# Optimization experiments

Measured on AMD Instinct MI355X. Metric: run time of the kernel, lower is better.

## Reference

```python
import jax, jax.numpy as jnp
import numpy as np

S = 4096
D_MODEL = 1024
D_INTERNAL = 4096


def setup_inputs() -> dict:
    key = jax.random.key(0)
    ks = jax.random.split(key, 12)
    s = 0.02
    return {
        "x": jax.random.normal(ks[0], (S, D_MODEL), dtype=jnp.float32),
        # projection weights stored as [d_in, d_out] so y = x @ W + b
        "Wq": jax.random.normal(ks[1], (D_MODEL, D_MODEL), dtype=jnp.float32) * s,
        "bq": jnp.zeros((D_MODEL,), dtype=jnp.float32),
        "Wk": jax.random.normal(ks[2], (D_MODEL, D_MODEL), dtype=jnp.float32) * s,
        "bk": jnp.zeros((D_MODEL,), dtype=jnp.float32),
        "Wv": jax.random.normal(ks[3], (D_MODEL, D_MODEL), dtype=jnp.float32) * s,
        "bv": jnp.zeros((D_MODEL,), dtype=jnp.float32),
        "W1": jax.random.normal(ks[4], (D_MODEL, D_INTERNAL), dtype=jnp.float32) * s,
        "b1": jnp.zeros((D_INTERNAL,), dtype=jnp.float32),
        "W2": jax.random.normal(ks[5], (D_INTERNAL, D_MODEL), dtype=jnp.float32) * s,
        "b2": jnp.zeros((D_MODEL,), dtype=jnp.float32),
    }


def reference(x, Wq, bq, Wk, bk, Wv, bv, W1, b1, W2, b2):
    # x: [S, D] (module is unbatched: k.transpose(0,1) implies 2-D input)
    d_model = x.shape[-1]
    q = x @ Wq + bq                         # [S, D]
    k = x @ Wk + bk                         # [S, D]
    v = x @ Wv + bv                         # [S, D]
    scores = (q @ k.T) / jnp.sqrt(jnp.asarray(d_model, x.dtype))  # [S, S]
    s = x.shape[0]
    causal = jnp.triu(jnp.ones((s, s), dtype=bool), k=1)           # True above diag
    scores = jnp.where(causal, jnp.asarray(-1e9, x.dtype), scores)
    attn = jax.nn.softmax(scores, axis=-1)  # [S, S]
    attended = attn @ v                     # [S, D]
    h = x + attended                        # residual 1
    ff = jax.nn.relu(h @ W1 + b1) @ W2 + b2 # 2-layer MLP
    out = h + ff                            # residual 2
    return (out, attn)
```

## Files before the change

### kernel.cpp

```cpp
#include <hip/hip_runtime.h>
#include <hip/hip_bf16.h>


typedef __attribute__((ext_vector_type(4))) float  f32x4;
typedef __attribute__((ext_vector_type(8))) short  bf16x8;
typedef __attribute__((ext_vector_type(4))) unsigned short us4;
typedef __attribute__((ext_vector_type(8))) unsigned short us8;

#define DEVINL __device__ __forceinline__

static constexpr int S   = 4096;
static constexpr int DM  = 1024;
static constexpr int DI  = 4096;

DEVINL unsigned short f2bf(float f) {
  union { float f; unsigned u; } v; v.f = f;
  unsigned r = v.u + 0x7fffu + ((v.u >> 16) & 1u);
  return (unsigned short)(r >> 16);
}

DEVINL float bf2f(unsigned short b) {
  union { unsigned u; float f; } v; v.u = ((unsigned)b) << 16;
  return v.f;
}

DEVINL void gld_lds16(const unsigned short* g, unsigned short* l) {
  __builtin_amdgcn_global_load_lds(
      (const __attribute__((address_space(1))) void*)g,
      (__attribute__((address_space(3))) void*)l,
      16, 0, 0);
}

DEVINL int xcd_remap(int orig, int nwg) {
  const int q = nwg >> 3, r = nwg & 7;
  const int x = orig & 7, idx = orig >> 3;
  return (x < r ? x * (q + 1) : r * (q + 1) + (x - r) * q) + idx;
}

__global__ void cvt_f32_bf16(const float* __restrict__ in,
                             unsigned short* __restrict__ out, long n) {
  long i = ((long)blockIdx.x * 256 + threadIdx.x) * 8;
  if (i >= n) return;
  f32x4 a = *(const f32x4*)(in + i);
  f32x4 b = *(const f32x4*)(in + i + 4);
  us8 o;
  o[0] = f2bf(a[0]); o[1] = f2bf(a[1]); o[2] = f2bf(a[2]); o[3] = f2bf(a[3]);
  o[4] = f2bf(b[0]); o[5] = f2bf(b[1]); o[6] = f2bf(b[2]); o[7] = f2bf(b[3]);
  *(us8*)(out + i) = o;
}

__global__ void transpose_cvt(const float* __restrict__ in,
                              unsigned short* __restrict__ out, int R, int C) {
  __shared__ float tile[32][33];
  const int bx = blockIdx.x * 32, by = blockIdx.y * 32;
  const int tx = threadIdx.x, ty = threadIdx.y;
  #pragma unroll
  for (int j = 0; j < 4; ++j) {
    int r = ty + j * 8;
    tile[r][tx] = in[(size_t)(by + r) * C + bx + tx];
  }
  __syncthreads();
  #pragma unroll
  for (int j = 0; j < 4; ++j) {
    int r = ty + j * 8;
    out[(size_t)(bx + r) * R + by + tx] = f2bf(tile[tx][r]);
  }
}

__global__ void transpose_bf16(const unsigned short* __restrict__ in, int ld,
                               unsigned short* __restrict__ out, int ldo) {
  __shared__ unsigned short tile[32][33];
  const int bx = blockIdx.x * 32, by = blockIdx.y * 32;
  const int tx = threadIdx.x, ty = threadIdx.y;
  #pragma unroll
  for (int j = 0; j < 4; ++j) {
    int r = ty + j * 8;
    tile[r][tx] = in[(size_t)(by + r) * ld + bx + tx];
  }
  __syncthreads();
  #pragma unroll
  for (int j = 0; j < 4; ++j) {
    int r = ty + j * 8;
    out[(size_t)(bx + r) * ldo + by + tx] = tile[tx][r];
  }
}

enum { EPI_QKV = 0, EPI_SCE = 1, EPI_FF1 = 4, EPI_PART = 6 };

#define VM_WAIT4 asm volatile("s_waitcnt vmcnt(4)" ::: "memory")
#define VM_WAIT0 asm volatile("s_waitcnt vmcnt(0)" ::: "memory")

template <int EPI, bool TRI_PACK, bool TRI_TRUNC>
__launch_bounds__(256, 3)
__global__ void gemm4(const unsigned short* __restrict__ A,
                      const unsigned short* __restrict__ Bt,
                      int M, int N, int K, int lda, int ldb, int kChunk, int GX,
                      const float* __restrict__ bias,
                      float* __restrict__ Cf,
                      unsigned short* __restrict__ Cb,
                      float scale) {
  const int wgid = xcd_remap(blockIdx.x, gridDim.x);
  int bm, bn;
  if (TRI_PACK) {
    int t = wgid;
    bm = (int)((sqrtf(8.f * (float)t + 1.f) - 1.f) * 0.5f);
    while ((bm + 1) * (bm + 2) / 2 <= t) ++bm;
    while (bm * (bm + 1) / 2 > t) --bm;
    bn = t - bm * (bm + 1) / 2;
  } else { bm = wgid / GX; bn = wgid % GX; }
  const int bm0 = bm * 128, bn0 = bn * 128;

  const int kbeg = blockIdx.z * kChunk;
  int kend = min(K, kbeg + kChunk);
  if (TRI_TRUNC) kend = min(kend, bm0 + 128);
  const int len = kend - kbeg;
  const int NT = (len > 0) ? (len >> 5) : 0;

  __shared__ __align__(16) unsigned short lds[3 * 8192];

  const int tid  = threadIdx.x;
  const int lane = tid & 63;
  const int w    = tid >> 6;
  const int wr   = w >> 1, wc = w & 1;
  const int fr   = lane & 15, fq = lane >> 4;

  f32x4 acc[4][4] = {};

  const int tq = tid >> 2;
  const int swcolE = ((tid & 3) * 8) ^ ((tq & 6) << 2);
  const unsigned short* gA = A  + (size_t)(bm0 + tq) * lda + kbeg + swcolE;
  const unsigned short* gB = Bt + (size_t)(bn0 + tq) * ldb + kbeg + swcolE;
  const size_t aH = (size_t)64 * lda, bH = (size_t)64 * ldb;

  auto stage = [&](int slot, int t_) {
    unsigned short* base = (unsigned short*)lds + slot * 8192;
    const size_t go = (size_t)t_ * 32;
    gld_lds16(gA + go,      base + w * 512);
    gld_lds16(gA + aH + go, base + 2048 + w * 512);
    gld_lds16(gB + go,      base + 4096 + w * 512);
    gld_lds16(gB + bH + go, base + 6144 + w * 512);
  };

  const int frSw = (fq * 8) ^ ((fr & 6) << 2);
  auto rdA = [&](int slot, int mi) {
    return *(const bf16x8*)((const unsigned short*)lds + slot * 8192 +
                            (wr * 64 + mi * 16 + fr) * 32 + frSw);
  };
  auto rdB = [&](int slot, int ni) {
    return *(const bf16x8*)((const unsigned short*)lds + slot * 8192 + 4096 +
                            (wc * 64 + ni * 16 + fr) * 32 + frSw);
  };

  if (NT > 0) {
    stage(0, 0);
    if (NT > 1) { stage(1, 1); VM_WAIT4; } else { VM_WAIT0; }
    __builtin_amdgcn_s_barrier();

    int slot = 0;
    for (int t = 0; t < NT; ++t) {
      const bool pf2 = (t + 2 < NT);
      if (pf2) {
        int s2 = slot + 2; if (s2 >= 3) s2 -= 3;
        stage(s2, t + 2);
      }

      bf16x8 a[4], b[4];
      #pragma unroll
      for (int mi = 0; mi < 4; ++mi) a[mi] = rdA(slot, mi);
      #pragma unroll
      for (int ni = 0; ni < 4; ++ni) b[ni] = rdB(slot, ni);
      #pragma unroll
      for (int mi = 0; mi < 4; ++mi)
        #pragma unroll
        for (int ni = 0; ni < 4; ++ni)
          acc[mi][ni] = __builtin_amdgcn_mfma_f32_16x16x32_bf16(
              a[mi], b[ni], acc[mi][ni], 0, 0, 0);

      if (t + 1 < NT) {
        if (pf2) { VM_WAIT4; } else { VM_WAIT0; }
        __builtin_amdgcn_s_barrier();
      }
      ++slot; if (slot >= 3) slot -= 3;
    }
  }

  const int row0 = bm0 + wr * 64 + fq * 4;
  const int col0 = bn0 + wc * 64 + fr;
  const size_t zoff = (EPI == EPI_PART) ? (size_t)blockIdx.z * M * N : 0;
  #pragma unroll
  for (int ni = 0; ni < 4; ++ni) {
    const int col = col0 + ni * 16;
    float bval = 0.f;
    if (EPI == EPI_QKV || EPI == EPI_FF1) bval = bias[col];
    #pragma unroll
    for (int mi = 0; mi < 4; ++mi) {
      #pragma unroll
      for (int j = 0; j < 4; ++j) {
        const int row = row0 + mi * 16 + j;
        const size_t idx = zoff + (size_t)row * N + col;
        const float c = acc[mi][ni][j];
        if (EPI == EPI_QKV) {
          Cb[idx] = f2bf(c + bval);
        } else if (EPI == EPI_SCE) {
          const float e = (col <= row) ? __expf(c * scale) : 0.f;
          Cb[idx] = f2bf(e);
        } else if (EPI == EPI_FF1) {
          const float r = c + bval;
          Cb[idx] = f2bf(r > 0.f ? r : 0.f);
        } else {
          Cf[idx] = c;
        }
      }
    }
  }
}

__global__ void normalize_rows(const unsigned short* __restrict__ attnb,
                               float* __restrict__ attnf,
                               float* __restrict__ rowsum) {
  const int m = blockIdx.x;
  const int tid = threadIdx.x;
  const int valid = m + 1;
  const unsigned short* rowb = attnb + (size_t)m * S;
  float* rowf = attnf + (size_t)m * S;

  float v[4][4];
  float lsum = 0.f;
  #pragma unroll
  for (int i = 0; i < 4; ++i) {
    const int idx = tid * 4 + i * 1024;
    #pragma unroll
    for (int j = 0; j < 4; ++j) v[i][j] = 0.f;
    if (i * 1024 <= m) {
      us4 b = *(const us4*)(rowb + idx);
      #pragma unroll
      for (int j = 0; j < 4; ++j) {
        const float e = (idx + j < valid) ? bf2f(b[j]) : 0.f;
        v[i][j] = e;
        lsum += e;
      }
    }
  }
  #pragma unroll
  for (int off = 32; off > 0; off >>= 1)
    lsum += __shfl_xor(lsum, off, 64);

  __shared__ float red[4];
  if ((tid & 63) == 0) red[tid >> 6] = lsum;
  __syncthreads();
  const float total = red[0] + red[1] + red[2] + red[3];
  if (tid == 0) rowsum[m] = total;
  const float inv = 1.0f / total;

  #pragma unroll
  for (int i = 0; i < 4; ++i) {
    const int idx = tid * 4 + i * 1024;
    f32x4 o;
    #pragma unroll
    for (int j = 0; j < 4; ++j) o[j] = v[i][j] * inv;
    *(f32x4*)(rowf + idx) = o;
  }
}

template <bool FINAL, bool NORM>
__global__ void reduce_k(const float* __restrict__ P,
                         const float* __restrict__ res,
                         const float* __restrict__ bias,
                         const float* __restrict__ rowsum,
                         float* __restrict__ outf,
                         unsigned short* __restrict__ outb, long n) {
  long i = ((long)blockIdx.x * 256 + threadIdx.x) * 4;
  if (i >= n) return;
  f32x4 a = *(const f32x4*)(P + i);
  f32x4 b = *(const f32x4*)(P + n + i);
  f32x4 r = *(const f32x4*)(res + i);
  float inv = 1.f;
  if (NORM) inv = 1.0f / rowsum[i >> 10];
  if (FINAL) {
    f32x4 bb = *(const f32x4*)(bias + (i & (DM - 1)));
    f32x4 o;
    #pragma unroll
    for (int j = 0; j < 4; ++j) o[j] = a[j] + b[j] + r[j] + bb[j];
    *(f32x4*)(outf + i) = o;
  } else {
    f32x4 o; us4 ob;
    #pragma unroll
    for (int j = 0; j < 4; ++j) {
      o[j] = (a[j] + b[j]) * inv + r[j];
      ob[j] = f2bf(o[j]);
    }
    *(f32x4*)(outf + i) = o;
    *(us4*)(outb + i) = ob;
  }
}

extern "C" void kernel_launch(void* const* d_in, const int* in_sizes, int n_in,
                              void* d_out, int out_size, void* d_ws, size_t ws_size,
                              hipStream_t stream) {
  const float* x  = (const float*)d_in[0];
  const float* Wq = (const float*)d_in[1];
  const float* bq = (const float*)d_in[2];
  const float* Wk = (const float*)d_in[3];
  const float* bk = (const float*)d_in[4];
  const float* Wv = (const float*)d_in[5];
  const float* bv = (const float*)d_in[6];
  const float* W1 = (const float*)d_in[7];
  const float* b1 = (const float*)d_in[8];
  const float* W2 = (const float*)d_in[9];
  const float* b2 = (const float*)d_in[10];
  (void)in_sizes; (void)n_in; (void)out_size; (void)ws_size;

  float* outp  = (float*)d_out;
  float* attnf = (float*)d_out + (size_t)S * DM;

  const size_t MB = 1ull << 20;
  char* ws = (char*)d_ws;
  unsigned short* W2t   = (unsigned short*)(ws + 0 * MB);
  unsigned short* W1t   = (unsigned short*)(ws + 8 * MB);
  float*          h     = (float*)(ws + 16 * MB);
  unsigned short* hb    = (unsigned short*)(ws + 32 * MB);
  unsigned short* vt    = (unsigned short*)(ws + 40 * MB);
  unsigned short* attnb = (unsigned short*)(ws + 48 * MB);
  unsigned short* qkv   = (unsigned short*)(ws + 80 * MB);
  unsigned short* xb    = (unsigned short*)(ws + 104 * MB);
  unsigned short* Wqkvt = (unsigned short*)(ws + 112 * MB);
  float*          bqkv  = (float*)(ws + 118 * MB);
  float*          rowsum= (float*)(ws + 119 * MB);
  unsigned short* ff1b  = (unsigned short*)(ws + 40 * MB);
  float*          Ppv   = (float*)(ws + 80 * MB);
  float*          Pff   = (float*)(ws + 72 * MB);

  cvt_f32_bf16<<<dim3((S * DM) / 2048), 256, 0, stream>>>(x, xb, (long)S * DM);
  transpose_cvt<<<dim3(DM / 32, DM / 32), dim3(32, 8), 0, stream>>>(Wq, Wqkvt, DM, DM);
  transpose_cvt<<<dim3(DM / 32, DM / 32), dim3(32, 8), 0, stream>>>(Wk, Wqkvt + (size_t)DM * DM, DM, DM);
  transpose_cvt<<<dim3(DM / 32, DM / 32), dim3(32, 8), 0, stream>>>(Wv, Wqkvt + 2 * (size_t)DM * DM, DM, DM);
  transpose_cvt<<<dim3(DI / 32, DM / 32), dim3(32, 8), 0, stream>>>(W1, W1t, DM, DI);
  transpose_cvt<<<dim3(DM / 32, DI / 32), dim3(32, 8), 0, stream>>>(W2, W2t, DI, DM);
  hipMemcpyAsync(bqkv,          bq, DM * sizeof(float), hipMemcpyDeviceToDevice, stream);
  hipMemcpyAsync(bqkv + DM,     bk, DM * sizeof(float), hipMemcpyDeviceToDevice, stream);
  hipMemcpyAsync(bqkv + 2 * DM, bv, DM * sizeof(float), hipMemcpyDeviceToDevice, stream);

  gemm4<EPI_QKV, false, false><<<dim3((S / 128) * (3072 / 128), 1, 1), 256, 0, stream>>>(
      xb, Wqkvt, S, 3072, DM, DM, DM, DM, 3072 / 128, bqkv, nullptr, qkv, 1.f);
  transpose_bf16<<<dim3(DM / 32, S / 32), dim3(32, 8), 0, stream>>>(
      qkv + 2 * DM, 3072, vt, S);

  gemm4<EPI_SCE, true, false><<<dim3(528, 1, 1), 256, 0, stream>>>(
      qkv, qkv + DM, S, S, DM, 3072, 3072, DM, 0, nullptr, nullptr, attnb, 0.03125f);

  normalize_rows<<<dim3(S), 256, 0, stream>>>(attnb, attnf, rowsum);

  gemm4<EPI_PART, false, true><<<dim3((S / 128) * (DM / 128), 1, 2), 256, 0, stream>>>(
      attnb, vt, S, DM, S, S, S, S / 2, DM / 128, nullptr, Ppv, nullptr, 1.f);
  reduce_k<false, true><<<dim3((S * DM) / 1024), 256, 0, stream>>>(
      Ppv, x, nullptr, rowsum, h, hb, (long)S * DM);

  gemm4<EPI_FF1, false, false><<<dim3((S / 128) * (DI / 128), 1, 1), 256, 0, stream>>>(
      hb, W1t, S, DI, DM, DM, DM, DM, DI / 128, b1, nullptr, ff1b, 1.f);

  gemm4<EPI_PART, false, false><<<dim3((S / 128) * (DM / 128), 1, 2), 256, 0, stream>>>(
      ff1b, W2t, S, DM, DI, DI, DI, DI / 2, DM / 128, nullptr, Pff, nullptr, 1.f);
  reduce_k<true, false><<<dim3((S * DM) / 1024), 256, 0, stream>>>(
      Pff, h, b2, nullptr, outp, nullptr, (long)S * DM);
}
```

Before: 269.4 us.

## Fuse prep kernels, use panel tile order, shrink GEMM to double buffer

Merges the x conversion, the five weight transpose-converts and the three bias copies into one prep kernel, removing eight launches and three memcpys. The GEMM non-triangular tile mapping becomes panel-major: groups of 8 column tiles are swept across all row tiles, aimed at better L2 reuse of B. The GEMM pipeline also drops from three LDS buffers to two, with a full vmcnt(0) wait and barrier every iteration. The smaller LDS footprint may raise occupancy, but prefetch depth drops to one tile, which can expose global-load latency.

```diff
diff --git a/kernel.cpp b/kernel.cpp
--- a/kernel.cpp
+++ b/kernel.cpp
@@ -37,23 +37,51 @@
   return (x < r ? x * (q + 1) : r * (q + 1) + (x - r) * q) + idx;
 }
 
-__global__ void cvt_f32_bf16(const float* __restrict__ in,
-                             unsigned short* __restrict__ out, long n) {
-  long i = ((long)blockIdx.x * 256 + threadIdx.x) * 8;
-  if (i >= n) return;
-  f32x4 a = *(const f32x4*)(in + i);
-  f32x4 b = *(const f32x4*)(in + i + 4);
-  us8 o;
-  o[0] = f2bf(a[0]); o[1] = f2bf(a[1]); o[2] = f2bf(a[2]); o[3] = f2bf(a[3]);
-  o[4] = f2bf(b[0]); o[5] = f2bf(b[1]); o[6] = f2bf(b[2]); o[7] = f2bf(b[3]);
-  *(us8*)(out + i) = o;
-}
-
-__global__ void transpose_cvt(const float* __restrict__ in,
-                              unsigned short* __restrict__ out, int R, int C) {
+__global__ void prep_all(const float* __restrict__ x,
+                         const float* __restrict__ Wq,
+                         const float* __restrict__ Wk,
+                         const float* __restrict__ Wv,
+                         const float* __restrict__ W1,
+                         const float* __restrict__ W2,
+                         const float* __restrict__ bq,
+                         const float* __restrict__ bk,
+                         const float* __restrict__ bv,
+                         unsigned short* __restrict__ xb,
+                         unsigned short* __restrict__ Wqkvt,
+                         unsigned short* __restrict__ W1t,
+                         unsigned short* __restrict__ W2t,
+                         float* __restrict__ bqkv) {
   __shared__ float tile[32][33];
-  const int bx = blockIdx.x * 32, by = blockIdx.y * 32;
-  const int tx = threadIdx.x, ty = threadIdx.y;
+  const int b = blockIdx.x;
+  const int tid = threadIdx.x;
+
+  if (b < 2048) {
+    long i = ((long)b * 256 + tid) * 8;
+    f32x4 a = *(const f32x4*)(x + i);
+    f32x4 c = *(const f32x4*)(x + i + 4);
+    us8 o;
+    o[0] = f2bf(a[0]); o[1] = f2bf(a[1]); o[2] = f2bf(a[2]); o[3] = f2bf(a[3]);
+    o[4] = f2bf(c[0]); o[5] = f2bf(c[1]); o[6] = f2bf(c[2]); o[7] = f2bf(c[3]);
+    *(us8*)(xb + i) = o;
+    return;
+  }
+  if (b >= 13312) {
+    const int t = b - 13312;
+    const float* src = (t == 0) ? bq : (t == 1) ? bk : bv;
+    const int i = tid * 4;
+    *(f32x4*)(bqkv + t * DM + i) = *(const f32x4*)(src + i);
+    return;
+  }
+
+  const float* in; unsigned short* out; int R, C, t;
+  if (b < 3072)      { in = Wq; out = Wqkvt;                      R = DM; C = DM; t = b - 2048; }
+  else if (b < 4096) { in = Wk; out = Wqkvt + (size_t)DM * DM;    R = DM; C = DM; t = b - 3072; }
+  else if (b < 5120) { in = Wv; out = Wqkvt + 2 * (size_t)DM * DM;R = DM; C = DM; t = b - 4096; }
+  else if (b < 9216) { in = W1; out = W1t;                        R = DM; C = DI; t = b - 5120; }
+  else               { in = W2; out = W2t;                        R = DI; C = DM; t = b - 9216; }
+  const int gx = C >> 5;
+  const int bx = (t % gx) * 32, by = (t / gx) * 32;
+  const int tx = tid & 31, ty = tid >> 5;
   #pragma unroll
   for (int j = 0; j < 4; ++j) {
     int r = ty + j * 8;
@@ -87,7 +115,6 @@
 
 enum { EPI_QKV = 0, EPI_SCE = 1, EPI_FF1 = 4, EPI_PART = 6 };
 
-#define VM_WAIT4 asm volatile("s_waitcnt vmcnt(4)" ::: "memory")
 #define VM_WAIT0 asm volatile("s_waitcnt vmcnt(0)" ::: "memory")
 
 template <int EPI, bool TRI_PACK, bool TRI_TRUNC>
@@ -99,15 +126,21 @@
                       float* __restrict__ Cf,
                       unsigned short* __restrict__ Cb,
                       float scale) {
-  const int wgid = xcd_remap(blockIdx.x, gridDim.x);
+  const int wg = xcd_remap(blockIdx.x, gridDim.x);
   int bm, bn;
   if (TRI_PACK) {
-    int t = wgid;
+    int t = wg;
     bm = (int)((sqrtf(8.f * (float)t + 1.f) - 1.f) * 0.5f);
     while ((bm + 1) * (bm + 2) / 2 <= t) ++bm;
     while (bm * (bm + 1) / 2 > t) --bm;
     bn = t - bm * (bm + 1) / 2;
-  } else { bm = wgid / GX; bn = wgid % GX; }
+  } else {
+    const int GY_ = gridDim.x / GX;
+    const int bpp = GY_ * 8;
+    const int panel = wg / bpp, rem = wg % bpp;
+    bm = rem >> 3;
+    bn = panel * 8 + (rem & 7);
+  }
   const int bm0 = bm * 128, bn0 = bn * 128;
 
   const int kbeg = blockIdx.z * kChunk;
@@ -116,7 +149,7 @@
   const int len = kend - kbeg;
   const int NT = (len > 0) ? (len >> 5) : 0;
 
-  __shared__ __align__(16) unsigned short lds[3 * 8192];
+  __shared__ __align__(16) unsigned short lds[2 * 8192];
 
   const int tid  = threadIdx.x;
   const int lane = tid & 63;
@@ -132,8 +165,8 @@
   const unsigned short* gB = Bt + (size_t)(bn0 + tq) * ldb + kbeg + swcolE;
   const size_t aH = (size_t)64 * lda, bH = (size_t)64 * ldb;
 
-  auto stage = [&](int slot, int t_) {
-    unsigned short* base = (unsigned short*)lds + slot * 8192;
+  auto stage = [&](int buf, int t_) {
+    unsigned short* base = (unsigned short*)lds + buf * 8192;
     const size_t go = (size_t)t_ * 32;
     gld_lds16(gA + go,      base + w * 512);
     gld_lds16(gA + aH + go, base + 2048 + w * 512);
@@ -142,33 +175,30 @@
   };
 
   const int frSw = (fq * 8) ^ ((fr & 6) << 2);
-  auto rdA = [&](int slot, int mi) {
-    return *(const bf16x8*)((const unsigned short*)lds + slot * 8192 +
+  auto rdA = [&](int buf, int mi) {
+    return *(const bf16x8*)((const unsigned short*)lds + buf * 8192 +
                             (wr * 64 + mi * 16 + fr) * 32 + frSw);
   };
-  auto rdB = [&](int slot, int ni) {
-    return *(const bf16x8*)((const unsigned short*)lds + slot * 8192 + 4096 +
+  auto rdB = [&](int buf, int ni) {
+    return *(const bf16x8*)((const unsigned short*)lds + buf * 8192 + 4096 +
                             (wc * 64 + ni * 16 + fr) * 32 + frSw);
   };
 
   if (NT > 0) {
     stage(0, 0);
-    if (NT > 1) { stage(1, 1); VM_WAIT4; } else { VM_WAIT0; }
+    VM_WAIT0;
     __builtin_amdgcn_s_barrier();
 
-    int slot = 0;
     for (int t = 0; t < NT; ++t) {
-      const bool pf2 = (t + 2 < NT);
-      if (pf2) {
-        int s2 = slot + 2; if (s2 >= 3) s2 -= 3;
-        stage(s2, t + 2);
-      }
+      const int cur = t & 1, nxt = cur ^ 1;
+      const bool pf = (t + 1 < NT);
+      if (pf) stage(nxt, t + 1);
 
       bf16x8 a[4], b[4];
       #pragma unroll
-      for (int mi = 0; mi < 4; ++mi) a[mi] = rdA(slot, mi);
-      #pragma unroll
-      for (int ni = 0; ni < 4; ++ni) b[ni] = rdB(slot, ni);
+      for (int mi = 0; mi < 4; ++mi) a[mi] = rdA(cur, mi);
+      #pragma unroll
+      for (int ni = 0; ni < 4; ++ni) b[ni] = rdB(cur, ni);
       #pragma unroll
       for (int mi = 0; mi < 4; ++mi)
         #pragma unroll
@@ -176,11 +206,8 @@
           acc[mi][ni] = __builtin_amdgcn_mfma_f32_16x16x32_bf16(
               a[mi], b[ni], acc[mi][ni], 0, 0, 0);
 
-      if (t + 1 < NT) {
-        if (pf2) { VM_WAIT4; } else { VM_WAIT0; }
-        __builtin_amdgcn_s_barrier();
-      }
-      ++slot; if (slot >= 3) slot -= 3;
+      if (pf) { VM_WAIT0; }
+      __builtin_amdgcn_s_barrier();
     }
   }
 
@@ -330,15 +357,8 @@
   float*          Ppv   = (float*)(ws + 80 * MB);
   float*          Pff   = (float*)(ws + 72 * MB);
 
-  cvt_f32_bf16<<<dim3((S * DM) / 2048), 256, 0, stream>>>(x, xb, (long)S * DM);
-  transpose_cvt<<<dim3(DM / 32, DM / 32), dim3(32, 8), 0, stream>>>(Wq, Wqkvt, DM, DM);
-  transpose_cvt<<<dim3(DM / 32, DM / 32), dim3(32, 8), 0, stream>>>(Wk, Wqkvt + (size_t)DM * DM, DM, DM);
-  transpose_cvt<<<dim3(DM / 32, DM / 32), dim3(32, 8), 0, stream>>>(Wv, Wqkvt + 2 * (size_t)DM * DM, DM, DM);
-  transpose_cvt<<<dim3(DI / 32, DM / 32), dim3(32, 8), 0, stream>>>(W1, W1t, DM, DI);
-  transpose_cvt<<<dim3(DM / 32, DI / 32), dim3(32, 8), 0, stream>>>(W2, W2t, DI, DM);
-  hipMemcpyAsync(bqkv,          bq, DM * sizeof(float), hipMemcpyDeviceToDevice, stream);
-  hipMemcpyAsync(bqkv + DM,     bk, DM * sizeof(float), hipMemcpyDeviceToDevice, stream);
-  hipMemcpyAsync(bqkv + 2 * DM, bv, DM * sizeof(float), hipMemcpyDeviceToDevice, stream);
+  prep_all<<<dim3(13315), 256, 0, stream>>>(
+      x, Wq, Wk, Wv, W1, W2, bq, bk, bv, xb, Wqkvt, W1t, W2t, bqkv);
 
   gemm4<EPI_QKV, false, false><<<dim3((S / 128) * (3072 / 128), 1, 1), 256, 0, stream>>>(
       xb, Wqkvt, S, 3072, DM, DM, DM, DM, 3072 / 128, bqkv, nullptr, qkv, 1.f);
```

New measurement: 247.0 us. 1.09x faster.
